# Kernel tuning notes

Hardware: AMD Instinct MI355X
Metric: run time of the kernel (lower is better)

## Reference

```python
import jax, jax.numpy as jnp
import numpy as np

B, NUM, NVAR = 2048, 100, 11
NUM_OBS, NC = 10, 3
T_FIN = 10.0
RHO_OBS = 1.0; RHO_INEQ = 1.0; RHO_LANE = 1.0; RHO_PROJ = 1.0
W_SMOOTH = 20.0; W_VDES = 2.0; W_YDES = 1.0
A_EGO = 3.0; B_EGO = 1.5; MARGIN = 0.2
V_MIN = 0.001; V_MAX = 18.0; A_MAX = 6.0
MAXITER = 5
H = 256

def _basis():
    s = np.linspace(0.0, 1.0, NUM)
    j = np.arange(NVAR)
    P = s[:, None] ** j[None, :]
    Pd = np.zeros((NUM, NVAR)); Pdd = np.zeros((NUM, NVAR))
    Pd[:, 1:] = j[1:][None, :] * s[:, None] ** (j[1:] - 1)[None, :]
    Pdd[:, 2:] = (j[2:] * (j[2:] - 1))[None, :] * s[:, None] ** (j[2:] - 2)[None, :]
    return (jnp.asarray(P, jnp.float32), jnp.asarray(Pd / T_FIN, jnp.float32),
            jnp.asarray(Pdd / (T_FIN ** 2), jnp.float32))

P, PDOT, PDDOT = _basis()
A_EQ_X = jnp.stack([P[0], PDOT[0], PDDOT[0], P[-1]])   # [4, NVAR]
A_EQ_Y = jnp.stack([P[0], PDOT[0], PDDOT[0]])          # [3, NVAR]
PTP = P.T @ P

def _kkt_inv(Q, A):
    m = A.shape[0]
    K = jnp.concatenate([jnp.concatenate([Q, A.T], axis=1),
                         jnp.concatenate([A, jnp.zeros((m, m), jnp.float32)], axis=1)], axis=0)
    return jnp.linalg.inv(K)

# ADMM cost: rho_proj*I + smoothness + rho_obs*A_obs^T A_obs + rho_ineq*(Pdot^T Pdot + Pddot^T Pddot)
Q_COMMON = (RHO_PROJ + W_SMOOTH) * jnp.eye(NVAR, dtype=jnp.float32) \
    + RHO_OBS * NUM_OBS * NC * PTP \
    + RHO_INEQ * (PDOT.T @ PDOT + PDDOT.T @ PDDOT)
KKT_X = _kkt_inv(Q_COMMON, A_EQ_X)
KKT_Y = _kkt_inv(Q_COMMON + 2.0 * RHO_LANE * PTP, A_EQ_Y)   # A_lane = [P; -P]
# x_init QP (smoothness + v_des / y_des tracking)
Q_IX = W_SMOOTH * jnp.eye(NVAR, dtype=jnp.float32) + W_VDES * (PDOT.T @ PDOT)
KKT_IX = _kkt_inv(Q_IX, A_EQ_X)
KKT_IY = _kkt_inv(Q_IX + W_YDES * PTP, A_EQ_Y)


def _forward(init_state_ego, goal_des, closest_obs, psi_obs, dim_x_obs, dim_y_obs,
             y_ub, y_lb, gru_W_ih, gru_W_hh, gru_b, gru_h0,
             mlp_W1, mlp_b1, mlp_W2, mlp_b2):
    b = init_state_ego.shape[0]
    x0, y0, vx0, vy0, ax0, ay0 = (init_state_ego[:, i] for i in range(6))
    b_eq_x = jnp.stack([x0, vx0, ax0, goal_des[:, 0]], axis=1)   # [B,4]
    b_eq_y = jnp.stack([y0, vy0, ay0], axis=1)                    # [B,3]

    # ---- obstacle circle trajectories (static obstacles, vx=vy=0) ----
    xo = closest_obs[:, :NUM_OBS]; yo = closest_obs[:, NUM_OBS:2 * NUM_OBS]   # [B,O]
    r = jnp.stack([jnp.zeros_like(dim_x_obs),
                   (dim_x_obs - dim_y_obs) / 2,
                   -(dim_x_obs - dim_y_obs) / 2], axis=2)                      # [B,O,3]
    x_circ = xo[:, :, None] + r * jnp.cos(psi_obs)[:, :, None]                # [B,O,3]
    y_circ = yo[:, :, None] + r * jnp.sin(psi_obs)[:, :, None]
    shape4 = (b, NUM_OBS, NC, NUM)
    x_obs_f = jnp.broadcast_to(x_circ[..., None], shape4).reshape(b, -1)      # [B,O*C*T]
    y_obs_f = jnp.broadcast_to(y_circ[..., None], shape4).reshape(b, -1)
    rad = dim_y_obs / 2
    a_obs = jnp.broadcast_to((A_EGO + rad + MARGIN)[:, :, None, None], shape4).reshape(b, -1)
    b_obs = jnp.broadcast_to((B_EGO + rad + MARGIN)[:, :, None, None], shape4).reshape(b, -1)

    # ---- GRU context over obstacles -> learned lambda init ----
    feats = jnp.stack([xo, yo, dim_x_obs, dim_y_obs, psi_obs], axis=2)        # [B,O,5]
    def gru_step(h, x):
        gx = x @ gru_W_ih + gru_b
        gh = h @ gru_W_hh
        z = jax.nn.sigmoid(gx[:, :H] + gh[:, :H])
        rg = jax.nn.sigmoid(gx[:, H:2 * H] + gh[:, H:2 * H])
        n = jnp.tanh(gx[:, 2 * H:] + rg * gh[:, 2 * H:])
        return (1.0 - z) * n + z * h, None
    hT, _ = jax.lax.scan(gru_step, jnp.broadcast_to(gru_h0, (b, H)), jnp.swapaxes(feats, 0, 1))
    lam = jax.nn.relu(hT @ mlp_W1 + mlp_b1) @ mlp_W2 + mlp_b2                 # [B,2*NVAR]
    lam_x, lam_y = lam[:, :NVAR], lam[:, NVAR:]

    # ---- x_init: equality-constrained smoothness/tracking QP ----
    v_des = jnp.sqrt(vx0 ** 2 + vy0 ** 2)
    lin_ix = W_VDES * v_des[:, None] * jnp.sum(PDOT, axis=0)[None, :]
    lin_iy = W_YDES * goal_des[:, 1:2] * jnp.sum(P, axis=0)[None, :]
    c_x0 = (jnp.concatenate([lin_ix, b_eq_x], 1) @ KKT_IX.T)[:, :NVAR]
    c_y0 = (jnp.concatenate([lin_iy, b_eq_y], 1) @ KKT_IY.T)[:, :NVAR]

    b_lane = jnp.concatenate([y_ub[:, None] * jnp.ones((1, NUM), jnp.float32),
                              -y_lb[:, None] * jnp.ones((1, NUM), jnp.float32)], axis=1)  # [B,2T]

    def AobsT(v):   # A_obs^T v, v: [B, O*C*T] -> [B, NVAR]
        return v.reshape(b, NUM_OBS * NC, NUM).sum(axis=1) @ P

    def step(carry, _):
        c_x, c_y, lx, ly = carry
        x = c_x @ P.T; xd = c_x @ PDOT.T; xdd = c_x @ PDDOT.T
        y = c_y @ P.T; yd = c_y @ PDOT.T; ydd = c_y @ PDDOT.T
        wc = jnp.tile(x, (1, NUM_OBS * NC)) - x_obs_f
        ws = jnp.tile(y, (1, NUM_OBS * NC)) - y_obs_f
        alpha_o = jnp.arctan2(ws * a_obs, wc * b_obs)
        ca, sa = jnp.cos(alpha_o), jnp.sin(alpha_o)
        c1 = RHO_OBS * (a_obs ** 2 * ca ** 2 + b_obs ** 2 * sa ** 2)
        c2 = RHO_OBS * (a_obs * wc * ca + b_obs * ws * sa)
        d_o = jnp.maximum(1.0, c2 / c1)
        alpha_v = jnp.clip(jnp.arctan2(yd, xd), -0.41, 0.41)
        cv, sv = jnp.cos(alpha_v), jnp.sin(alpha_v)
        d_v = jnp.clip(xd * cv + yd * sv, V_MIN, V_MAX)
        alpha_a = jnp.arctan2(ydd + 1e-4, xdd + 1e-4)
        caa, saa = jnp.cos(alpha_a), jnp.sin(alpha_a)
        d_a = jnp.clip(xdd * caa + ydd * saa, 0.0, A_MAX)
        # targets
        b_ox = x_obs_f + a_obs * d_o * ca; b_oy = y_obs_f + b_obs * d_o * sa
        b_vx = d_v * cv; b_vy = d_v * sv
        b_ax = d_a * caa; b_ay = d_a * saa
        b_lane_aug = jnp.minimum(jnp.concatenate([y, -y], 1), b_lane)  # slack-augmented
        top_x = lx + RHO_PROJ * c_x0 + RHO_OBS * AobsT(b_ox) + RHO_INEQ * (b_vx @ PDOT + b_ax @ PDDOT)
        top_y = ly + RHO_PROJ * c_y0 + RHO_OBS * AobsT(b_oy) + RHO_INEQ * (b_vy @ PDOT + b_ay @ PDDOT) \
            + RHO_LANE * ((b_lane_aug[:, :NUM] - b_lane_aug[:, NUM:]) @ P)
        c_xn = (jnp.concatenate([top_x, b_eq_x], 1) @ KKT_X.T)[:, :NVAR]
        c_yn = (jnp.concatenate([top_y, b_eq_y], 1) @ KKT_Y.T)[:, :NVAR]
        # residuals / Lagrange multiplier updates
        xn = c_xn @ P.T; yn = c_yn @ P.T
        res_ox = jnp.tile(xn, (1, NUM_OBS * NC)) - b_ox
        res_oy = jnp.tile(yn, (1, NUM_OBS * NC)) - b_oy
        lxn = lx - RHO_OBS * AobsT(res_ox) \
            - RHO_INEQ * ((c_xn @ PDOT.T - b_vx) @ PDOT + (c_xn @ PDDOT.T - b_ax) @ PDDOT)
        res_lane = jnp.concatenate([yn, -yn], 1) - b_lane_aug
        lyn = ly - RHO_OBS * AobsT(res_oy) \
            - RHO_INEQ * ((c_yn @ PDOT.T - b_vy) @ PDOT + (c_yn @ PDDOT.T - b_ay) @ PDDOT) \
            - RHO_LANE * ((res_lane[:, :NUM] - res_lane[:, NUM:]) @ P)
        return (c_xn, c_yn, lxn, lyn), None

    (c_x, c_y, lam_x, lam_y), _ = jax.lax.scan(step, (c_x0, c_y0, lam_x, lam_y),
                                               None, length=MAXITER)
    return jnp.concatenate([c_x, c_y], axis=1)   # [B, 2*NVAR]


def setup_inputs() -> dict:
    key = jax.random.key(0)
    ks = jax.random.split(key, 12)
    d = {
        'init_state_ego': jax.random.normal(ks[0], (B, 6), jnp.float32),
        'goal_des': jax.random.normal(ks[1], (B, 2), jnp.float32),
        'closest_obs': jax.random.normal(ks[2], (B, 2 * NUM_OBS), jnp.float32),
        'psi_obs': jax.random.normal(ks[3], (B, NUM_OBS), jnp.float32),
        'dim_x_obs': jax.random.uniform(ks[4], (B, NUM_OBS), jnp.float32),
        'dim_y_obs': jax.random.uniform(ks[5], (B, NUM_OBS), jnp.float32),
        'y_ub': jnp.ones((B,), jnp.float32),
        'y_lb': jnp.zeros((B,), jnp.float32),
        'gru_W_ih': jax.random.normal(ks[6], (5, 3 * H), jnp.float32) / np.sqrt(5.0),
        'gru_W_hh': jax.random.normal(ks[7], (H, 3 * H), jnp.float32) / np.sqrt(float(H)),
        'gru_b': jnp.zeros((3 * H,), jnp.float32),
        'gru_h0': jax.random.normal(ks[8], (H,), jnp.float32) * 0.1,
        'mlp_W1': jax.random.normal(ks[9], (H, 512), jnp.float32) / np.sqrt(float(H)),
        'mlp_b1': jnp.zeros((512,), jnp.float32),
        'mlp_W2': jax.random.normal(ks[10], (512, 2 * NVAR), jnp.float32) / np.sqrt(512.0),
        'mlp_b2': jnp.zeros((2 * NVAR,), jnp.float32),
    }
    return d


def reference(init_state_ego, goal_des, closest_obs, psi_obs, dim_x_obs, dim_y_obs,
              y_ub, y_lb, gru_W_ih, gru_W_hh, gru_b, gru_h0,
              mlp_W1, mlp_b1, mlp_W2, mlp_b2):
    return _forward(init_state_ego, goal_des, closest_obs, psi_obs, dim_x_obs, dim_y_obs,
                    y_ub, y_lb, gru_W_ih, gru_W_hh, gru_b, gru_h0,
                    mlp_W1, mlp_b1, mlp_W2, mlp_b2)
```

## Files before the change

### kernel.cpp

```cpp
#include <hip/hip_runtime.h>
#include <math.h>

typedef short bf16x8 __attribute__((ext_vector_type(8)));
typedef float f32x4 __attribute__((ext_vector_type(4)));

__device__ __forceinline__ unsigned short f2bf(float x) {
  union { float f; unsigned u; } v; v.f = x;
  unsigned r = v.u + 0x7FFFu + ((v.u >> 16) & 1u);
  return (unsigned short)(r >> 16);
}
__device__ __forceinline__ float bf2f(unsigned short h) {
  union { unsigned u; float f; } v; v.u = ((unsigned)h) << 16; return v.f;
}

#define WS_WAUG  0u
#define WS_W1T   442368u
#define WS_HAUGA 704512u
#define WS_HAUGB 1884160u
#define WS_HF32  3063808u
#define WS_ACTS  3063808u
#define WS_LAM   5160960u
#define WS_KKT   5341184u
#define WS_SUMS  5344000u

__global__ __launch_bounds__(256) void prep(
    const float* __restrict__ Whh, const float* __restrict__ Wih,
    const float* __restrict__ gb, const float* __restrict__ W1,
    const float* __restrict__ h0,
    const float* __restrict__ obs, const float* __restrict__ dimx,
    const float* __restrict__ dimy, const float* __restrict__ psi,
    unsigned short* __restrict__ Waug, unsigned short* __restrict__ W1T,
    unsigned short* __restrict__ HaugA, unsigned short* __restrict__ HaugB,
    float* __restrict__ kkt_out, float* __restrict__ sums_out)
{
  __shared__ double S[21];
  __shared__ double aug[15][32];
  __shared__ double fbuf[15];
  if (blockIdx.x < 4) {
    const int mat = blockIdx.x;
    const int n = (mat == 0 || mat == 2) ? 15 : 14;
    const int twoN = 2 * n;
    if (threadIdx.x == 0) {
      for (int m = 0; m < 21; ++m) S[m] = 0.0;
      for (int s = 0; s < 100; ++s) {
        double t = s * (1.0 / 99.0);
        double p = 1.0;
        for (int m = 0; m < 21; ++m) { S[m] += p; p *= t; }
      }
    }
    __syncthreads();
    for (int idx = threadIdx.x; idx < n * twoN; idx += 256) {
      int r = idx / twoN, c = idx % twoN;
      double v;
      if (c >= n) v = (c - n == r) ? 1.0 : 0.0;
      else if (r < 11 && c < 11) {
        double ptp = S[r + c];
        double pdp = (r >= 1 && c >= 1) ? ((double)(r * c) / 100.0) * S[r + c - 2] : 0.0;
        double pddp = (r >= 2 && c >= 2) ? ((double)(r*(r-1)) * (double)(c*(c-1)) / 10000.0) * S[r + c - 4] : 0.0;
        double dg = (r == c) ? 1.0 : 0.0;
        if (mat == 0)      v = 21.0*dg + 30.0*ptp + pdp + pddp;
        else if (mat == 1) v = 21.0*dg + 32.0*ptp + pdp + pddp;
        else if (mat == 2) v = 20.0*dg + 2.0*pdp;
        else               v = 20.0*dg + 2.0*pdp + ptp;
      } else if (r >= 11 && c >= 11) v = 0.0;
      else {
        int ar = (r >= 11) ? (r - 11) : (c - 11);
        int ac = (r >= 11) ? c : r;
        v = (ar == 0) ? ((ac == 0) ? 1.0 : 0.0)
          : (ar == 1) ? ((ac == 1) ? 0.1 : 0.0)
          : (ar == 2) ? ((ac == 2) ? 0.02 : 0.0)
          : 1.0;
      }
      aug[r][c] = v;
    }
    __syncthreads();
    for (int p = 0; p < n; ++p) {
      double pv = aug[p][p];
      __syncthreads();
      double inv = 1.0 / pv;
      for (int c = threadIdx.x; c < twoN; c += 256) aug[p][c] *= inv;
      __syncthreads();
      if (threadIdx.x < n) fbuf[threadIdx.x] = aug[threadIdx.x][p];
      __syncthreads();
      for (int idx = threadIdx.x; idx < n * twoN; idx += 256) {
        int r = idx / twoN, c = idx % twoN;
        if (r != p) aug[r][c] -= fbuf[r] * aug[p][c];
      }
      __syncthreads();
    }
    for (int idx = threadIdx.x; idx < 11 * n; idx += 256) {
      int r = idx / n, c = idx % n;
      kkt_out[mat * 176 + r * 16 + c] = (float)aug[r][n + c];
    }
    if (mat == 0 && threadIdx.x < 11) {
      int j = threadIdx.x;
      sums_out[j] = (float)S[j];
      sums_out[11 + j] = (j >= 1) ? (float)((double)j / 10.0 * S[j - 1]) : 0.f;
    }
    return;
  }
  int idx = (blockIdx.x - 4) * 256 + threadIdx.x;
  if (idx < 221184) {
    int col = idx / 288, k = idx - col * 288;
    float v;
    if (k < 256)       v = Whh[k * 768 + col];
    else if (k < 261)  v = Wih[(k - 256) * 768 + col];
    else if (k == 261) v = gb[col];
    else               v = 0.f;
    Waug[idx] = f2bf(v);
  } else if (idx < 352256) {
    int j = idx - 221184;
    int col = j >> 8, k = j & 255;
    W1T[j] = f2bf(W1[k * 512 + col]);
  } else {
    int j = idx - 352256;
    unsigned short* dst = HaugA;
    if (j >= 589824) { j -= 589824; dst = HaugB; }
    int row = j / 288, k = j - row * 288;
    float v;
    if (k < 256)       v = h0[k];
    else if (k == 256) v = obs[row * 20 + 0];
    else if (k == 257) v = obs[row * 20 + 10];
    else if (k == 258) v = dimx[row * 10 + 0];
    else if (k == 259) v = dimy[row * 10 + 0];
    else if (k == 260) v = psi[row * 10 + 0];
    else if (k == 261) v = 1.0f;
    else               v = 0.f;
    dst[row * 288 + k] = f2bf(v);
  }
}

#define MFMA __builtin_amdgcn_mfma_f32_16x16x32_bf16
__global__ __launch_bounds__(256) void gru_step(
    const unsigned short* __restrict__ Waug,
    const unsigned short* __restrict__ HaugC, unsigned short* __restrict__ HaugN,
    float* __restrict__ Hf32, const float* __restrict__ h0,
    const float* __restrict__ obs, const float* __restrict__ dimx,
    const float* __restrict__ dimy, const float* __restrict__ psi,
    int s)
{
  __shared__ __align__(16) unsigned short LDSall[36864];
  const int tid = threadIdx.x;
  const int m0 = blockIdx.x * 32;
  const int c0 = blockIdx.y * 32;
  const int lane = tid & 63, w = tid >> 6;
  const int l15 = lane & 15, g4 = lane >> 4;

  #pragma unroll 4
  for (int r = 0; r < 18; ++r) {
    int j = tid + 256 * r;
    int tile = j >> 6, q = j & 63;
    int ci = q >> 2, ks = q & 3;
    const unsigned short* src;
    if (tile < 54) {
      int gate = tile / 18, rem = tile - gate * 18;
      int cg = rem / 9, kc = rem - cg * 9;
      int col = gate * 256 + c0 + cg * 16 + ci;
      src = Waug + (size_t)col * 288 + kc * 32 + ks * 8;
    } else {
      int t2 = tile - 54;
      int mi = t2 / 9, kc = t2 - mi * 9;
      int row = m0 + mi * 16 + ci;
      src = HaugC + (size_t)row * 288 + kc * 32 + ks * 8;
    }
    *(int4*)&LDSall[tile * 512 + q * 8] = *(const int4*)src;
  }
  __syncthreads();

  const int mi = w >> 1, cg = w & 1;
  const int foff = (l15 * 4 + g4) * 8;
  f32x4 accz = {0.f,0.f,0.f,0.f}, accr = {0.f,0.f,0.f,0.f};
  f32x4 anh = {0.f,0.f,0.f,0.f}, anx = {0.f,0.f,0.f,0.f};
  const unsigned short* As = &LDSall[54 * 512];

  #pragma unroll
  for (int kc = 0; kc < 9; ++kc) {
    bf16x8 a  = *(const bf16x8*)&As[(mi * 9 + kc) * 512 + foff];
    bf16x8 bz = *(const bf16x8*)&LDSall[((0 * 2 + cg) * 9 + kc) * 512 + foff];
    bf16x8 br = *(const bf16x8*)&LDSall[((1 * 2 + cg) * 9 + kc) * 512 + foff];
    bf16x8 bn = *(const bf16x8*)&LDSall[((2 * 2 + cg) * 9 + kc) * 512 + foff];
    accz = MFMA(a, bz, accz, 0, 0, 0);
    accr = MFMA(a, br, accr, 0, 0, 0);
    if (kc < 8) anh = MFMA(a, bn, anh, 0, 0, 0);
    else        anx = MFMA(a, bn, anx, 0, 0, 0);
  }

  const int colh = c0 + cg * 16 + l15;
  float h0c = (s == 0) ? h0[colh] : 0.f;
  #pragma unroll
  for (int rg = 0; rg < 4; ++rg) {
    int row = m0 + mi * 16 + g4 * 4 + rg;
    float hold = (s == 0) ? h0c : Hf32[(size_t)row * 256 + colh];
    float z = 1.f / (1.f + __expf(-accz[rg]));
    float rr = 1.f / (1.f + __expf(-accr[rg]));
    float nn = tanhf(anx[rg] + rr * anh[rg]);
    float hnew = (1.f - z) * nn + z * hold;
    Hf32[(size_t)row * 256 + colh] = hnew;
    HaugN[(size_t)row * 288 + colh] = f2bf(hnew);
  }
  if (blockIdx.y == 0 && s < 9 && tid < 192) {
    int row = m0 + tid / 6, e = tid - (tid / 6) * 6;
    int s1 = s + 1;
    float v = (e == 0) ? obs[row * 20 + s1] : (e == 1) ? obs[row * 20 + 10 + s1]
            : (e == 2) ? dimx[row * 10 + s1] : (e == 3) ? dimy[row * 10 + s1]
            : (e == 4) ? psi[row * 10 + s1] : 1.0f;
    HaugN[(size_t)row * 288 + 256 + e] = f2bf(v);
  }
}

__global__ __launch_bounds__(256) void mlp1(
    const unsigned short* __restrict__ Haug, const unsigned short* __restrict__ W1T,
    const float* __restrict__ b1, unsigned short* __restrict__ acts)
{
  __shared__ __align__(16) unsigned short As[8192];
  const int tid = threadIdx.x;
  const int m0 = blockIdx.x * 32, c0 = blockIdx.y * 128;
  const int lane = tid & 63, w = tid >> 6, l15 = lane & 15, g4 = lane >> 4;

  #pragma unroll
  for (int r = 0; r < 4; ++r) {
    int j = tid + 256 * r;
    int tile = j >> 6, q = j & 63, ci = q >> 2, ks = q & 3;
    int mi = tile >> 3, kc = tile & 7;
    const unsigned short* src = Haug + (size_t)(m0 + mi * 16 + ci) * 288 + kc * 32 + ks * 8;
    *(int4*)&As[tile * 512 + q * 8] = *(const int4*)src;
  }
  __syncthreads();

  const int foff = (l15 * 4 + g4) * 8;
  f32x4 acc[2][2];
  #pragma unroll
  for (int a = 0; a < 2; ++a)
    #pragma unroll
    for (int b = 0; b < 2; ++b) acc[a][b] = (f32x4){0.f,0.f,0.f,0.f};

  #pragma unroll
  for (int kc = 0; kc < 8; ++kc) {
    bf16x8 a0 = *(const bf16x8*)&As[(0 * 8 + kc) * 512 + foff];
    bf16x8 a1 = *(const bf16x8*)&As[(1 * 8 + kc) * 512 + foff];
    int kk = kc * 32 + g4 * 8;
    #pragma unroll
    for (int nt = 0; nt < 2; ++nt) {
      int col = c0 + w * 32 + nt * 16 + l15;
      bf16x8 b = *(const bf16x8*)&W1T[(size_t)col * 256 + kk];
      acc[0][nt] = MFMA(a0, b, acc[0][nt], 0, 0, 0);
      acc[1][nt] = MFMA(a1, b, acc[1][nt], 0, 0, 0);
    }
  }
  #pragma unroll
  for (int mi = 0; mi < 2; ++mi)
    #pragma unroll
    for (int nt = 0; nt < 2; ++nt) {
      int col = c0 + w * 32 + nt * 16 + l15;
      float bb = b1[col];
      #pragma unroll
      for (int rg = 0; rg < 4; ++rg) {
        int row = m0 + mi * 16 + g4 * 4 + rg;
        float v = fmaxf(acc[mi][nt][rg] + bb, 0.f);
        acts[(size_t)row * 512 + col] = f2bf(v);
      }
    }
}

__global__ __launch_bounds__(256) void mlp2(
    const unsigned short* __restrict__ acts, const float* __restrict__ W2,
    const float* __restrict__ b2, float* __restrict__ lam)
{
  __shared__ unsigned short Ablk[8 * 520];
  __shared__ float W2s[512 * 22];
  const int tid = threadIdx.x;
  const int m0 = blockIdx.x * 8;
  for (int i = tid; i < 4096; i += 256) {
    int r = i >> 9, k = i & 511;
    Ablk[r * 520 + k] = acts[(size_t)(m0 + r) * 512 + k];
  }
  for (int i = tid; i < 11264; i += 256) W2s[i] = W2[i];
  __syncthreads();
  if (tid < 176) {
    int row = tid / 22, col = tid - (tid / 22) * 22;
    float s = b2[col];
    const unsigned short* ap = &Ablk[row * 520];
    for (int k = 0; k < 512; ++k) s += bf2f(ap[k]) * W2s[k * 22 + col];
    lam[(size_t)(m0 + row) * 22 + col] = s;
  }
}

__global__ __launch_bounds__(128) void solver(
    const float* __restrict__ ise, const float* __restrict__ goal,
    const float* __restrict__ obs, const float* __restrict__ psi,
    const float* __restrict__ dimx, const float* __restrict__ dimy,
    const float* __restrict__ yub, const float* __restrict__ ylb,
    const float* __restrict__ lam, const float* __restrict__ kkt,
    const float* __restrict__ sums, float* __restrict__ out)
{
  __shared__ __align__(16) float Pt[3][11][108];
  __shared__ __align__(16) float red[7][108];
  __shared__ float redout[7][11];
  __shared__ float cx[11], cy[11], lx[11], ly[11], cx0[11], cy0[11];
  __shared__ float cxn[11], cyn[11];
  __shared__ float rhsx[15], rhsy[14];
  __shared__ float xc[30], yc[30], sa_[10], sb_[10], sab[10], sab2[10];

  const int b = blockIdx.x;
  const int tid = threadIdx.x;

  if (tid < 100) {
    float t = tid * (1.0f / 99.0f);
    float tjm2 = 0.f, tjm1 = 0.f, tj = 1.f;
    #pragma unroll
    for (int j = 0; j < 11; ++j) {
      Pt[0][j][tid] = tj;
      Pt[1][j][tid] = 0.1f * (float)j * tjm1;
      Pt[2][j][tid] = 0.01f * (float)(j * (j - 1)) * tjm2;
      tjm2 = tjm1; tjm1 = tj; tj *= t;
    }
  }
  if (tid < 10) {
    int o = tid;
    float xo = obs[b * 20 + o], yo = obs[b * 20 + 10 + o];
    float dx = dimx[b * 10 + o], dy = dimy[b * 10 + o], ps = psi[b * 10 + o];
    float sp, cp;
    __sincosf(ps, &sp, &cp);
    float r1 = 0.5f * (dx - dy);
    xc[o * 3] = xo; xc[o * 3 + 1] = xo + r1 * cp; xc[o * 3 + 2] = xo - r1 * cp;
    yc[o * 3] = yo; yc[o * 3 + 1] = yo + r1 * sp; yc[o * 3 + 2] = yo - r1 * sp;
    float rad = 0.5f * dy;
    float av = 3.2f + rad, bv = 1.7f + rad;
    sa_[o] = av; sb_[o] = bv; sab[o] = av * bv; sab2[o] = av * bv * av * bv;
  }
  if (tid < 11) { lx[tid] = lam[b * 22 + tid]; ly[tid] = lam[b * 22 + 11 + tid]; }
  const float vx0 = ise[b * 6 + 2], vy0 = ise[b * 6 + 3];
  if (tid == 0) {
    float x0 = ise[b * 6 + 0], y0 = ise[b * 6 + 1];
    float ax0 = ise[b * 6 + 4], ay0 = ise[b * 6 + 5];
    rhsx[11] = x0; rhsx[12] = vx0; rhsx[13] = ax0; rhsx[14] = goal[b * 2 + 0];
    rhsy[11] = y0; rhsy[12] = vy0; rhsy[13] = ay0;
  }
  {
    float vdes = sqrtf(vx0 * vx0 + vy0 * vy0);
    float gy = goal[b * 2 + 1];
    if (tid < 11) { rhsx[tid] = 2.f * vdes * sums[11 + tid]; rhsy[tid] = gy * sums[tid]; }
  }
  const float yU = yub[b], yL = ylb[b];
  __syncthreads();
  if (tid < 11) {
    const float* K = kkt + 2 * 176 + tid * 16;
    float s = 0.f;
    #pragma unroll
    for (int j = 0; j < 15; ++j) s += K[j] * rhsx[j];
    cx0[tid] = s; cx[tid] = s;
  } else if (tid >= 16 && tid < 27) {
    int i = tid - 16;
    const float* K = kkt + 3 * 176 + i * 16;
    float s = 0.f;
    #pragma unroll
    for (int j = 0; j < 14; ++j) s += K[j] * rhsy[j];
    cy0[i] = s; cy[i] = s;
  }
  __syncthreads();

  float Sbx = 0.f, Sby = 0.f, bvx = 0.f, bvy = 0.f, bax = 0.f, bay = 0.f, lane_t = 0.f;
  for (int it = 0; it < 5; ++it) {
    if (tid < 100) {
      float t = tid * (1.0f / 99.0f);
      float x = 0, y = 0, xd = 0, yd = 0, xdd = 0, ydd = 0;
      {
        float tjm2 = 0, tjm1 = 0, tj = 1;
        #pragma unroll
        for (int j = 0; j < 11; ++j) {
          float cj = cx[j], dj = cy[j];
          x += cj * tj; y += dj * tj;
          float pd = 0.1f * (float)j * tjm1;
          xd += cj * pd; yd += dj * pd;
          float pdd = 0.01f * (float)(j * (j - 1)) * tjm2;
          xdd += cj * pdd; ydd += dj * pdd;
          tjm2 = tjm1; tjm1 = tj; tj *= t;
        }
      }
      Sbx = 0.f; Sby = 0.f;
      for (int oi = 0; oi < 10; ++oi) {
        float A = sa_[oi], B = sb_[oi], AB = sab[oi], AB2 = sab2[oi];
        #pragma unroll
        for (int cc = 0; cc < 3; ++cc) {
          int o = oi * 3 + cc;
          float xcc = xc[o], ycc = yc[o];
          float wc = x - xcc, wsv = y - ycc;
          float p = wsv * A, q = wc * B;
          float h2 = p * p + q * q;
          float rin = rsqrtf(h2 + 1e-20f);
          float sc = AB * rin;
          bool outside = h2 >= AB2;
          Sbx += outside ? x : fmaf(wc, sc, xcc);
          Sby += outside ? y : fmaf(wsv, sc, ycc);
        }
      }
      bool clipv = (xd <= 0.f) || (fabsf(yd) > xd * 0.43463135f);
      float cv, sv;
      if (clipv) { cv = 0.91712081f; sv = copysignf(0.39860934f, yd); }
      else { float ri = rsqrtf(fmaxf(xd * xd + yd * yd, 1e-24f)); cv = xd * ri; sv = yd * ri; }
      float dv = fminf(fmaxf(xd * cv + yd * sv, 0.001f), 18.f);
      bvx = dv * cv; bvy = dv * sv;
      float qa = xdd + 1e-4f, pa = ydd + 1e-4f;
      float ria = rsqrtf(pa * pa + qa * qa + 1e-30f);
      float caa = qa * ria, saa = pa * ria;
      float da = fminf(fmaxf(xdd * caa + ydd * saa, 0.f), 6.f);
      bax = da * caa; bay = da * saa;
      lane_t = fminf(y, yU) - fminf(-y, -yL);
      red[0][tid] = Sbx; red[1][tid] = Sby; red[2][tid] = bvx; red[3][tid] = bvy;
      red[4][tid] = bax; red[5][tid] = bay; red[6][tid] = lane_t;
    }
    __syncthreads();
    if (tid < 77) {
      int a = tid / 11, j = tid - a * 11;
      int wt = (a < 2) ? 0 : (a < 4) ? 1 : (a < 6) ? 2 : 0;
      const float4* rp = (const float4*)(&red[a][0]);
      const float4* wp = (const float4*)(&Pt[wt][j][0]);
      float s = 0.f;
      for (int k = 0; k < 25; ++k) {
        float4 rv = rp[k], wv = wp[k];
        s += rv.x * wv.x + rv.y * wv.y + rv.z * wv.z + rv.w * wv.w;
      }
      redout[a][j] = s;
    }
    __syncthreads();
    if (tid < 11) rhsx[tid] = lx[tid] + cx0[tid] + redout[0][tid] + redout[2][tid] + redout[4][tid];
    else if (tid >= 16 && tid < 27) {
      int j = tid - 16;
      rhsy[j] = ly[j] + cy0[j] + redout[1][j] + redout[3][j] + redout[5][j] + redout[6][j];
    }
    __syncthreads();
    if (tid < 11) {
      const float* K = kkt + tid * 16;
      float s = 0.f;
      #pragma unroll
      for (int j = 0; j < 15; ++j) s += K[j] * rhsx[j];
      cxn[tid] = s;
    } else if (tid >= 16 && tid < 27) {
      int i = tid - 16;
      const float* K = kkt + 176 + i * 16;
      float s = 0.f;
      #pragma unroll
      for (int j = 0; j < 14; ++j) s += K[j] * rhsy[j];
      cyn[i] = s;
    }
    __syncthreads();
    if (tid < 100) {
      float t = tid * (1.0f / 99.0f);
      float xn = 0, yn = 0, xdn = 0, ydn = 0, xddn = 0, yddn = 0;
      {
        float tjm2 = 0, tjm1 = 0, tj = 1;
        #pragma unroll
        for (int j = 0; j < 11; ++j) {
          float cj = cxn[j], dj = cyn[j];
          xn += cj * tj; yn += dj * tj;
          float pd = 0.1f * (float)j * tjm1;
          xdn += cj * pd; ydn += dj * pd;
          float pdd = 0.01f * (float)(j * (j - 1)) * tjm2;
          xddn += cj * pdd; yddn += dj * pdd;
          tjm2 = tjm1; tjm1 = tj; tj *= t;
        }
      }
      red[0][tid] = 30.f * xn - Sbx;
      red[1][tid] = xdn - bvx;
      red[2][tid] = xddn - bax;
      red[3][tid] = 30.f * yn - Sby;
      red[4][tid] = ydn - bvy;
      red[5][tid] = yddn - bay;
      red[6][tid] = 2.f * yn - lane_t;
    }
    __syncthreads();
    if (tid < 77) {
      int a = tid / 11, j = tid - a * 11;
      int wt = (a == 0 || a == 3 || a == 6) ? 0 : (a == 1 || a == 4) ? 1 : 2;
      const float4* rp = (const float4*)(&red[a][0]);
      const float4* wp = (const float4*)(&Pt[wt][j][0]);
      float s = 0.f;
      for (int k = 0; k < 25; ++k) {
        float4 rv = rp[k], wv = wp[k];
        s += rv.x * wv.x + rv.y * wv.y + rv.z * wv.z + rv.w * wv.w;
      }
      redout[a][j] = s;
    }
    __syncthreads();
    if (tid < 11) { lx[tid] -= redout[0][tid] + redout[1][tid] + redout[2][tid]; cx[tid] = cxn[tid]; }
    else if (tid >= 16 && tid < 27) {
      int j = tid - 16;
      ly[j] -= redout[3][j] + redout[4][j] + redout[5][j] + redout[6][j];
      cy[j] = cyn[j];
    }
    __syncthreads();
  }
  if (tid < 11) out[b * 22 + tid] = cx[tid];
  else if (tid >= 16 && tid < 27) out[b * 22 + 11 + (tid - 16)] = cy[tid - 16];
}

extern "C" void kernel_launch(void* const* d_in, const int* in_sizes, int n_in,
                              void* d_out, int out_size, void* d_ws, size_t ws_size,
                              hipStream_t stream) {
  const float* ise  = (const float*)d_in[0];
  const float* goal = (const float*)d_in[1];
  const float* obs  = (const float*)d_in[2];
  const float* psi  = (const float*)d_in[3];
  const float* dimx = (const float*)d_in[4];
  const float* dimy = (const float*)d_in[5];
  const float* yub  = (const float*)d_in[6];
  const float* ylb  = (const float*)d_in[7];
  const float* Wih  = (const float*)d_in[8];
  const float* Whh  = (const float*)d_in[9];
  const float* gb   = (const float*)d_in[10];
  const float* h0   = (const float*)d_in[11];
  const float* W1   = (const float*)d_in[12];
  const float* b1   = (const float*)d_in[13];
  const float* W2   = (const float*)d_in[14];
  const float* b2   = (const float*)d_in[15];

  char* ws = (char*)d_ws;
  unsigned short* Waug  = (unsigned short*)(ws + WS_WAUG);
  unsigned short* W1T   = (unsigned short*)(ws + WS_W1T);
  unsigned short* HaugA = (unsigned short*)(ws + WS_HAUGA);
  unsigned short* HaugB = (unsigned short*)(ws + WS_HAUGB);
  float* Hf32 = (float*)(ws + WS_HF32);
  unsigned short* acts = (unsigned short*)(ws + WS_ACTS);
  float* lamb = (float*)(ws + WS_LAM);
  float* kkt  = (float*)(ws + WS_KKT);
  float* sums = (float*)(ws + WS_SUMS);

  prep<<<5988, 256, 0, stream>>>(Whh, Wih, gb, W1, h0, obs, dimx, dimy, psi,
                                 Waug, W1T, HaugA, HaugB, kkt, sums);
  for (int s = 0; s < 10; ++s) {
    const unsigned short* hc = (s & 1) ? HaugB : HaugA;
    unsigned short* hn = (s & 1) ? HaugA : HaugB;
    gru_step<<<dim3(64, 8), 256, 0, stream>>>(Waug, hc, hn, Hf32, h0,
                                              obs, dimx, dimy, psi, s);
  }
  mlp1<<<dim3(64, 4), 256, 0, stream>>>(HaugA, W1T, b1, acts);
  mlp2<<<256, 256, 0, stream>>>(acts, W2, b2, lamb);
  solver<<<2048, 128, 0, stream>>>(ise, goal, obs, psi, dimx, dimy, yub, ylb,
                                   lamb, kkt, sums, (float*)d_out);
  (void)in_sizes; (void)n_in; (void)out_size; (void)ws_size;
}
```

Before: 266.3 us.

## Fold ADMM lambda update into precomputed matrices, drop LDS staging in GRU step

The solver's per-iteration second trajectory evaluation and its reduction pass are replaced by precomputed G = I - M*K and M matrices, built in double precision in prep. The lambda update then becomes a small 11x11 matvec on the same rhs used for the coefficient solve, which removes a sync-heavy reduction per ADMM iteration. Separately, gru_step now loads MFMA operands straight from global memory instead of staging them in LDS. The prep kernel also stops writing the full HaugB buffer and zeroes only its padding columns. The algebraic rewrite relies on the lambda update being exactly linear in the rhs, and float rounding may differ slightly from the original.

Result: faster. 245.3 us (-7.9%).

```diff
diff --git a/kernel.cpp b/kernel.cpp
--- a/kernel.cpp
+++ b/kernel.cpp
@@ -21,7 +21,11 @@
 #define WS_ACTS  3063808u
 #define WS_LAM   5160960u
 #define WS_KKT   5341184u
-#define WS_SUMS  5344000u
+#define WS_GX    5344000u
+#define WS_GY    5344704u
+#define WS_MX    5345408u
+#define WS_MY    5346112u
+#define WS_SUMS  5346816u
 
 __global__ __launch_bounds__(256) void prep(
     const float* __restrict__ Whh, const float* __restrict__ Wih,
@@ -31,11 +35,14 @@
     const float* __restrict__ dimy, const float* __restrict__ psi,
     unsigned short* __restrict__ Waug, unsigned short* __restrict__ W1T,
     unsigned short* __restrict__ HaugA, unsigned short* __restrict__ HaugB,
-    float* __restrict__ kkt_out, float* __restrict__ sums_out)
+    float* __restrict__ kkt_out, float* __restrict__ Gx_out,
+    float* __restrict__ Gy_out, float* __restrict__ Mx_out,
+    float* __restrict__ My_out, float* __restrict__ sums_out)
 {
   __shared__ double S[21];
   __shared__ double aug[15][32];
   __shared__ double fbuf[15];
+  __shared__ double Md[11][11];
   if (blockIdx.x < 4) {
     const int mat = blockIdx.x;
     const int n = (mat == 0 || mat == 2) ? 15 : 14;
@@ -92,6 +99,24 @@
       int r = idx / n, c = idx % n;
       kkt_out[mat * 176 + r * 16 + c] = (float)aug[r][n + c];
     }
+    if (mat < 2) {
+      if (threadIdx.x < 121) {
+        int j = threadIdx.x / 11, i = threadIdx.x % 11;
+        double m = 30.0 * S[j + i];
+        if (j >= 1 && i >= 1) m += ((double)(j * i) / 100.0) * S[j + i - 2];
+        if (j >= 2 && i >= 2) m += ((double)(j*(j-1)) * (double)(i*(i-1)) / 10000.0) * S[j + i - 4];
+        if (mat == 1) m += 2.0 * S[j + i];
+        Md[j][i] = m;
+      }
+      __syncthreads();
+      if (threadIdx.x < 121) {
+        int j = threadIdx.x / 11, i = threadIdx.x % 11;
+        double g = (j == i) ? 1.0 : 0.0;
+        for (int k = 0; k < 11; ++k) g -= Md[j][k] * aug[k][n + i];
+        if (mat == 0) { Gx_out[j * 16 + i] = (float)g; Mx_out[j * 16 + i] = (float)Md[j][i]; }
+        else          { Gy_out[j * 16 + i] = (float)g; My_out[j * 16 + i] = (float)Md[j][i]; }
+      }
+    }
     if (mat == 0 && threadIdx.x < 11) {
       int j = threadIdx.x;
       sums_out[j] = (float)S[j];
@@ -112,10 +137,8 @@
     int j = idx - 221184;
     int col = j >> 8, k = j & 255;
     W1T[j] = f2bf(W1[k * 512 + col]);
-  } else {
+  } else if (idx < 942080) {
     int j = idx - 352256;
-    unsigned short* dst = HaugA;
-    if (j >= 589824) { j -= 589824; dst = HaugB; }
     int row = j / 288, k = j - row * 288;
     float v;
     if (k < 256)       v = h0[k];
@@ -126,7 +149,11 @@
     else if (k == 260) v = psi[row * 10 + 0];
     else if (k == 261) v = 1.0f;
     else               v = 0.f;
-    dst[row * 288 + k] = f2bf(v);
+    HaugA[row * 288 + k] = f2bf(v);
+  } else if (idx < 995328) {
+    int j = idx - 942080;
+    int row = j / 26, k = 262 + (j - row * 26);
+    HaugB[row * 288 + k] = 0;
   }
 }
 
@@ -139,46 +166,25 @@
     const float* __restrict__ dimy, const float* __restrict__ psi,
     int s)
 {
-  __shared__ __align__(16) unsigned short LDSall[36864];
   const int tid = threadIdx.x;
   const int m0 = blockIdx.x * 32;
   const int c0 = blockIdx.y * 32;
   const int lane = tid & 63, w = tid >> 6;
   const int l15 = lane & 15, g4 = lane >> 4;
-
-  #pragma unroll 4
-  for (int r = 0; r < 18; ++r) {
-    int j = tid + 256 * r;
-    int tile = j >> 6, q = j & 63;
-    int ci = q >> 2, ks = q & 3;
-    const unsigned short* src;
-    if (tile < 54) {
-      int gate = tile / 18, rem = tile - gate * 18;
-      int cg = rem / 9, kc = rem - cg * 9;
-      int col = gate * 256 + c0 + cg * 16 + ci;
-      src = Waug + (size_t)col * 288 + kc * 32 + ks * 8;
-    } else {
-      int t2 = tile - 54;
-      int mi = t2 / 9, kc = t2 - mi * 9;
-      int row = m0 + mi * 16 + ci;
-      src = HaugC + (size_t)row * 288 + kc * 32 + ks * 8;
-    }
-    *(int4*)&LDSall[tile * 512 + q * 8] = *(const int4*)src;
-  }
-  __syncthreads();
-
   const int mi = w >> 1, cg = w & 1;
-  const int foff = (l15 * 4 + g4) * 8;
+
+  const unsigned short* Arow = HaugC + (size_t)(m0 + mi * 16 + l15) * 288 + g4 * 8;
+  const unsigned short* Bcol = Waug + (size_t)(c0 + cg * 16 + l15) * 288 + g4 * 8;
+
   f32x4 accz = {0.f,0.f,0.f,0.f}, accr = {0.f,0.f,0.f,0.f};
   f32x4 anh = {0.f,0.f,0.f,0.f}, anx = {0.f,0.f,0.f,0.f};
-  const unsigned short* As = &LDSall[54 * 512];
 
   #pragma unroll
   for (int kc = 0; kc < 9; ++kc) {
-    bf16x8 a  = *(const bf16x8*)&As[(mi * 9 + kc) * 512 + foff];
-    bf16x8 bz = *(const bf16x8*)&LDSall[((0 * 2 + cg) * 9 + kc) * 512 + foff];
-    bf16x8 br = *(const bf16x8*)&LDSall[((1 * 2 + cg) * 9 + kc) * 512 + foff];
-    bf16x8 bn = *(const bf16x8*)&LDSall[((2 * 2 + cg) * 9 + kc) * 512 + foff];
+    bf16x8 a  = *(const bf16x8*)(Arow + kc * 32);
+    bf16x8 bz = *(const bf16x8*)(Bcol + kc * 32);
+    bf16x8 br = *(const bf16x8*)(Bcol + 256 * 288 + kc * 32);
+    bf16x8 bn = *(const bf16x8*)(Bcol + 512 * 288 + kc * 32);
     accz = MFMA(a, bz, accz, 0, 0, 0);
     accr = MFMA(a, br, accr, 0, 0, 0);
     if (kc < 8) anh = MFMA(a, bn, anh, 0, 0, 0);
@@ -291,13 +297,15 @@
     const float* __restrict__ dimx, const float* __restrict__ dimy,
     const float* __restrict__ yub, const float* __restrict__ ylb,
     const float* __restrict__ lam, const float* __restrict__ kkt,
+    const float* __restrict__ Gxm, const float* __restrict__ Gym,
+    const float* __restrict__ Mxm, const float* __restrict__ Mym,
     const float* __restrict__ sums, float* __restrict__ out)
 {
   __shared__ __align__(16) float Pt[3][11][108];
   __shared__ __align__(16) float red[7][108];
   __shared__ float redout[7][11];
   __shared__ float cx[11], cy[11], lx[11], ly[11], cx0[11], cy0[11];
-  __shared__ float cxn[11], cyn[11];
+  __shared__ float kxB[11], kyB[11], hx[11], hy[11];
   __shared__ float rhsx[15], rhsy[14];
   __shared__ float xc[30], yc[30], sa_[10], sb_[10], sab[10], sab2[10];
 
@@ -349,6 +357,11 @@
     #pragma unroll
     for (int j = 0; j < 15; ++j) s += K[j] * rhsx[j];
     cx0[tid] = s; cx[tid] = s;
+    const float* Kx = kkt + tid * 16;
+    float kb = 0.f;
+    #pragma unroll
+    for (int c = 0; c < 4; ++c) kb += Kx[11 + c] * rhsx[11 + c];
+    kxB[tid] = kb;
   } else if (tid >= 16 && tid < 27) {
     int i = tid - 16;
     const float* K = kkt + 3 * 176 + i * 16;
@@ -356,10 +369,27 @@
     #pragma unroll
     for (int j = 0; j < 14; ++j) s += K[j] * rhsy[j];
     cy0[i] = s; cy[i] = s;
+    const float* Ky = kkt + 176 + i * 16;
+    float kb = 0.f;
+    #pragma unroll
+    for (int c = 0; c < 3; ++c) kb += Ky[11 + c] * rhsy[11 + c];
+    kyB[i] = kb;
   }
   __syncthreads();
-
-  float Sbx = 0.f, Sby = 0.f, bvx = 0.f, bvy = 0.f, bax = 0.f, bay = 0.f, lane_t = 0.f;
+  if (tid < 11) {
+    float s = cx0[tid];
+    #pragma unroll
+    for (int i = 0; i < 11; ++i) s += Mxm[tid * 16 + i] * kxB[i];
+    hx[tid] = s;
+  } else if (tid >= 16 && tid < 27) {
+    int j = tid - 16;
+    float s = cy0[j];
+    #pragma unroll
+    for (int i = 0; i < 11; ++i) s += Mym[j * 16 + i] * kyB[i];
+    hy[j] = s;
+  }
+  __syncthreads();
+
   for (int it = 0; it < 5; ++it) {
     if (tid < 100) {
       float t = tid * (1.0f / 99.0f);
@@ -377,7 +407,7 @@
           tjm2 = tjm1; tjm1 = tj; tj *= t;
         }
       }
-      Sbx = 0.f; Sby = 0.f;
+      float Sbx = 0.f, Sby = 0.f;
       for (int oi = 0; oi < 10; ++oi) {
         float A = sa_[oi], B = sb_[oi], AB = sab[oi], AB2 = sab2[oi];
         #pragma unroll
@@ -399,15 +429,14 @@
       if (clipv) { cv = 0.91712081f; sv = copysignf(0.39860934f, yd); }
       else { float ri = rsqrtf(fmaxf(xd * xd + yd * yd, 1e-24f)); cv = xd * ri; sv = yd * ri; }
       float dv = fminf(fmaxf(xd * cv + yd * sv, 0.001f), 18.f);
-      bvx = dv * cv; bvy = dv * sv;
       float qa = xdd + 1e-4f, pa = ydd + 1e-4f;
       float ria = rsqrtf(pa * pa + qa * qa + 1e-30f);
       float caa = qa * ria, saa = pa * ria;
       float da = fminf(fmaxf(xdd * caa + ydd * saa, 0.f), 6.f);
-      bax = da * caa; bay = da * saa;
-      lane_t = fminf(y, yU) - fminf(-y, -yL);
-      red[0][tid] = Sbx; red[1][tid] = Sby; red[2][tid] = bvx; red[3][tid] = bvy;
-      red[4][tid] = bax; red[5][tid] = bay; red[6][tid] = lane_t;
+      red[0][tid] = Sbx; red[1][tid] = Sby;
+      red[2][tid] = dv * cv; red[3][tid] = dv * sv;
+      red[4][tid] = da * caa; red[5][tid] = da * saa;
+      red[6][tid] = fminf(y, yU) - fminf(-y, -yL);
     }
     __syncthreads();
     if (tid < 77) {
@@ -416,6 +445,7 @@
       const float4* rp = (const float4*)(&red[a][0]);
       const float4* wp = (const float4*)(&Pt[wt][j][0]);
       float s = 0.f;
+      #pragma unroll
       for (int k = 0; k < 25; ++k) {
         float4 rv = rp[k], wv = wp[k];
         s += rv.x * wv.x + rv.y * wv.y + rv.z * wv.z + rv.w * wv.w;
@@ -431,62 +461,27 @@
     __syncthreads();
     if (tid < 11) {
       const float* K = kkt + tid * 16;
-      float s = 0.f;
+      const float* G = Gxm + tid * 16;
+      float sc = kxB[tid], sl = -hx[tid];
       #pragma unroll
-      for (int j = 0; j < 15; ++j) s += K[j] * rhsx[j];
-      cxn[tid] = s;
+      for (int i = 0; i < 11; ++i) {
+        float r = rhsx[i];
+        sc += K[i] * r;
+        sl += G[i] * r;
+      }
+      cx[tid] = sc; lx[tid] = sl;
     } else if (tid >= 16 && tid < 27) {
-      int i = tid - 16;
-      const float* K = kkt + 176 + i * 16;
-      float s = 0.f;
+      int j = tid - 16;
+      const float* K = kkt + 176 + j * 16;
+      const float* G = Gym + j * 16;
+      float sc = kyB[j], sl = -hy[j];
       #pragma unroll
-      for (int j = 0; j < 14; ++j) s += K[j] * rhsy[j];
-      cyn[i] = s;
-    }
-    __syncthreads();
-    if (tid < 100) {
-      float t = tid * (1.0f / 99.0f);
-      float xn = 0, yn = 0, xdn = 0, ydn = 0, xddn = 0, yddn = 0;
-      {
-        float tjm2 = 0, tjm1 = 0, tj = 1;
-        #pragma unroll
-        for (int j = 0; j < 11; ++j) {
-          float cj = cxn[j], dj = cyn[j];
-          xn += cj * tj; yn += dj * tj;
-          float pd = 0.1f * (float)j * tjm1;
-          xdn += cj * pd; ydn += dj * pd;
-          float pdd = 0.01f * (float)(j * (j - 1)) * tjm2;
-          xddn += cj * pdd; yddn += dj * pdd;
-          tjm2 = tjm1; tjm1 = tj; tj *= t;
-        }
-      }
-      red[0][tid] = 30.f * xn - Sbx;
-      red[1][tid] = xdn - bvx;
-      red[2][tid] = xddn - bax;
-      red[3][tid] = 30.f * yn - Sby;
-      red[4][tid] = ydn - bvy;
-      red[5][tid] = yddn - bay;
-      red[6][tid] = 2.f * yn - lane_t;
-    }
-    __syncthreads();
-    if (tid < 77) {
-      int a = tid / 11, j = tid - a * 11;
-      int wt = (a == 0 || a == 3 || a == 6) ? 0 : (a == 1 || a == 4) ? 1 : 2;
-      const float4* rp = (const float4*)(&red[a][0]);
-      const float4* wp = (const float4*)(&Pt[wt][j][0]);
-      float s = 0.f;
-      for (int k = 0; k < 25; ++k) {
-        float4 rv = rp[k], wv = wp[k];
-        s += rv.x * wv.x + rv.y * wv.y + rv.z * wv.z + rv.w * wv.w;
-      }
-      redout[a][j] = s;
-    }
-    __syncthreads();
-    if (tid < 11) { lx[tid] -= redout[0][tid] + redout[1][tid] + redout[2][tid]; cx[tid] = cxn[tid]; }
-    else if (tid >= 16 && tid < 27) {
-      int j = tid - 16;
-      ly[j] -= redout[3][j] + redout[4][j] + redout[5][j] + redout[6][j];
-      cy[j] = cyn[j];
+      for (int i = 0; i < 11; ++i) {
+        float r = rhsy[i];
+        sc += K[i] * r;
+        sl += G[i] * r;
+      }
+      cy[j] = sc; ly[j] = sl;
     }
     __syncthreads();
   }
@@ -523,10 +518,14 @@
   unsigned short* acts = (unsigned short*)(ws + WS_ACTS);
   float* lamb = (float*)(ws + WS_LAM);
   float* kkt  = (float*)(ws + WS_KKT);
+  float* Gxm  = (float*)(ws + WS_GX);
+  float* Gym  = (float*)(ws + WS_GY);
+  float* Mxm  = (float*)(ws + WS_MX);
+  float* Mym  = (float*)(ws + WS_MY);
   float* sums = (float*)(ws + WS_SUMS);
 
-  prep<<<5988, 256, 0, stream>>>(Whh, Wih, gb, W1, h0, obs, dimx, dimy, psi,
-                                 Waug, W1T, HaugA, HaugB, kkt, sums);
+  prep<<<3892, 256, 0, stream>>>(Whh, Wih, gb, W1, h0, obs, dimx, dimy, psi,
+                                 Waug, W1T, HaugA, HaugB, kkt, Gxm, Gym, Mxm, Mym, sums);
   for (int s = 0; s < 10; ++s) {
     const unsigned short* hc = (s & 1) ? HaugB : HaugA;
     unsigned short* hn = (s & 1) ? HaugA : HaugB;
@@ -536,6 +535,6 @@
   mlp1<<<dim3(64, 4), 256, 0, stream>>>(HaugA, W1T, b1, acts);
   mlp2<<<256, 256, 0, stream>>>(acts, W2, b2, lamb);
   solver<<<2048, 128, 0, stream>>>(ise, goal, obs, psi, dimx, dimy, yub, ylb,
-                                   lamb, kkt, sums, (float*)d_out);
+                                   lamb, kkt, Gxm, Gym, Mxm, Mym, sums, (float*)d_out);
   (void)in_sizes; (void)n_in; (void)out_size; (void)ws_size;
 }
```
